# Optimization experiments

Measured on AMD Instinct MI355X. Metric: run time of the kernel, lower is better.

## Reference

```python
import jax, jax.numpy as jnp
import numpy as np

T, B, L, CTX, H = 512, 512, 16, 64, 128
STATE_DIM, SHOT, PID, DATA = 32, 12, 35, 23


def setup_inputs() -> dict:
    key = jax.random.key(0)
    ks = jax.random.split(key, 64)
    k = iter(ks)
    def rn(shape, s=0.1):
        return (jax.random.normal(next(k), shape) * s).astype(jnp.float32)
    xs = jax.random.normal(next(k), (T, B, DATA), jnp.float32)
    xs = xs.at[:, :, 12].set(jax.random.randint(next(k), (T, B), 0, SHOT).astype(jnp.float32))
    xs = xs.at[:, :, 17].set(jax.random.randint(next(k), (T, B), 0, PID).astype(jnp.float32))
    xs = xs.at[:, :, 20].set(jax.random.randint(next(k), (T, B), 0, SHOT).astype(jnp.float32))
    return dict(
        total_xs=jnp.zeros((1,), jnp.float32),
        xs=xs,
        ts=jnp.linspace(0.0, 2.0, T).astype(jnp.float32),
        noise_std=jnp.asarray(0.1, jnp.float32),
        z0_noise=jax.random.normal(next(k), (B, L), jnp.float32),
        bm_noise=jax.random.normal(next(k), (T - 1, B, L), jnp.float32),
        shot_emb=rn((SHOT, 8)), player_emb=rn((PID, 8)),
        gru_wih=rn((3 * H, STATE_DIM)), gru_whh=rn((3 * H, H)),
        gru_bih=rn((3 * H,)), gru_bhh=rn((3 * H,)),
        enc_w=rn((CTX, H)), enc_b=rn((CTX,)),
        qz0_w=rn((2 * L, CTX)), qz0_b=rn((2 * L,)),
        f_w1=rn((H, L + CTX)), f_b1=rn((H,)), f_w2=rn((H, H)), f_b2=rn((H,)),
        f_w3=rn((L, H)), f_b3=rn((L,)),
        h_w1=rn((H, L)), h_b1=rn((H,)), h_w2=rn((H, H)), h_b2=rn((H,)),
        h_w3=rn((L, H)), h_b3=rn((L,)),
        g_w1=rn((L, H)), g_b1=rn((L, H)), g_w2=rn((L, H)), g_b2=rn((L,)),
        proj_w=rn((STATE_DIM, L)), proj_b=rn((STATE_DIM,)),
        pz0_mean=jnp.zeros((1, L), jnp.float32), pz0_logstd=jnp.zeros((1, L), jnp.float32),
        act_w=rn((128, L)), act_b=rn((128,)),
        act_land_w=rn((2, 128)), act_shot_w=rn((SHOT, 128)), act_move_w=rn((2, 128)),
    )


def _forward(xs, noise_std, shot_emb, player_emb, gru_wih, gru_whh, gru_bih, gru_bhh,
             enc_w, enc_b, qz0_w, qz0_b,
             f_w1, f_b1, f_w2, f_b2, f_w3, f_b3,
             h_w1, h_b1, h_w2, h_b2, h_w3, h_b3,
             g_w1, g_b1, g_w2, g_b2,
             proj_w, proj_b, pz0_mean, pz0_logstd,
             act_w, act_b, act_land_w, act_shot_w, act_move_w,
             ts, z0_noise, bm_noise):
    # --- SDE_embed_and_transform: replace shot/player id cols with embeddings ---
    state = xs[:, :, :18]
    shot_ids = state[:, :, 12].astype(jnp.int32)
    pid_ids = state[:, :, 17].astype(jnp.int32)
    state_t = jnp.concatenate([state[:, :, :12], shot_emb[shot_ids],
                               state[:, :, 13:17], player_emb[pid_ids]], axis=-1)  # (T,B,32)
    xs_t = jnp.concatenate([state_t, xs[:, :, 18:]], axis=-1)  # (T,B,37)
    # --- Encoder: GRU over time-reversed states, linear head, flip back ---
    def gru_step(h, xt):
        gi = xt @ gru_wih.T + gru_bih
        gh = h @ gru_whh.T + gru_bhh
        ir, iz, inn = jnp.split(gi, 3, axis=-1)
        hr, hz, hn = jnp.split(gh, 3, axis=-1)
        r = jax.nn.sigmoid(ir + hr)
        zg = jax.nn.sigmoid(iz + hz)
        n = jnp.tanh(inn + r * hn)
        hnew = (1.0 - zg) * n + zg * h
        return hnew, hnew
    h0 = jnp.zeros((xs.shape[1], gru_whh.shape[1]), xs.dtype)
    _, hs = jax.lax.scan(gru_step, h0, state_t[::-1])
    ctx = (hs @ enc_w.T + enc_b)[::-1]  # (T,B,CTX)
    # --- posterior z0 ---
    qm, qls = jnp.split(ctx[0] @ qz0_w.T + qz0_b, 2, axis=1)
    z0 = qm + jnp.exp(qls) * z0_noise
    # --- Euler-Maruyama with logqp; searchsorted(right) -> ctx[min(i+1,T-1)] = ctx[i+1] ---
    dts = ts[1:] - ts[:-1]  # (T-1,)
    dW = jnp.sqrt(dts)[:, None, None] * bm_noise
    ctx_steps = ctx[1:]
    def mlp3(x, w1, b1, w2, b2, w3, b3):
        h1 = jax.nn.softplus(x @ w1.T + b1)
        h2 = jax.nn.softplus(h1 @ w2.T + b2)
        return h2 @ w3.T + b3
    def g_diag(y):  # (B,L): per-latent-dim scalar nets, batched over L
        hg = jax.nn.softplus(y[:, :, None] * g_w1[None] + g_b1[None])  # (B,L,H)
        return jax.nn.sigmoid(jnp.einsum('blh,lh->bl', hg, g_w2) + g_b2)
    def sde_step(z, inp):
        c, dw, dt = inp
        f_val = mlp3(jnp.concatenate([z, c], axis=1), f_w1, f_b1, f_w2, f_b2, f_w3, f_b3)
        h_val = mlp3(z, h_w1, h_b1, h_w2, h_b2, h_w3, h_b3)
        g_val = g_diag(z)
        u = (f_val - h_val) / g_val
        logr = 0.5 * jnp.sum(u * u, axis=1) * dt
        z_new = z + f_val * dt + g_val * dw
        return z_new, (z_new, logr)
    _, (z_tail, log_ratio) = jax.lax.scan(sde_step, z0, (ctx_steps, dW, dts))
    zs = jnp.concatenate([z0[None], z_tail], axis=0)  # (T,B,L)
    _xs = zs @ proj_w.T + proj_b  # (T,B,32)
    # --- action model losses ---
    a = jax.nn.relu(zs @ act_w.T + act_b)
    land = (a @ act_land_w.T).reshape(-1, 2)
    shot_logits = (a @ act_shot_w.T).reshape(-1, act_shot_w.shape[0])
    move = (a @ act_move_w.T).reshape(-1, 2)
    true_actions = xs_t[:, :, -5:]
    true_land = true_actions[:, :, :2].reshape(-1, 2)
    true_move = true_actions[:, :, 3:].reshape(-1, 2)
    true_shot = true_actions[:, :, 2].astype(jnp.int32).reshape(-1)
    land_loss = jnp.mean((land - true_land) ** 2)
    move_loss = jnp.mean((move - true_move) ** 2)
    logp = jax.nn.log_softmax(shot_logits, axis=-1)
    picked = jnp.take_along_axis(logp, true_shot[:, None], axis=1)[:, 0]
    mask = (true_shot != 0).astype(logp.dtype)  # CrossEntropy ignore_index=0
    shot_loss = -jnp.sum(picked * mask) / jnp.maximum(jnp.sum(mask), 1.0)
    # --- reconstruction log-likelihood ---
    xs_state = xs_t[:, :, :STATE_DIM]
    LOG2PI = 1.8378770664093453
    log_pxs = jnp.mean(jnp.sum(
        -0.5 * ((xs_state - _xs) / noise_std) ** 2 - jnp.log(noise_std) - 0.5 * LOG2PI,
        axis=(0, 2)))
    # --- KL(q(z0) || p(z0)) ---
    var_q = jnp.exp(2.0 * qls)
    var_p = jnp.exp(2.0 * pz0_logstd)
    kl = pz0_logstd - qls + (var_q + (qm - pz0_mean) ** 2) / (2.0 * var_p) - 0.5
    logqp0 = jnp.mean(jnp.sum(kl, axis=1))
    logqp_path = jnp.mean(jnp.sum(log_ratio, axis=0))
    return log_pxs, logqp0 + logqp_path + land_loss + shot_loss + move_loss


def reference(total_xs, xs, ts, noise_std, z0_noise, bm_noise, shot_emb, player_emb,
              gru_wih, gru_whh, gru_bih, gru_bhh, enc_w, enc_b, qz0_w, qz0_b,
              f_w1, f_b1, f_w2, f_b2, f_w3, f_b3, h_w1, h_b1, h_w2, h_b2, h_w3, h_b3,
              g_w1, g_b1, g_w2, g_b2, proj_w, proj_b, pz0_mean, pz0_logstd,
              act_w, act_b, act_land_w, act_shot_w, act_move_w):
    return _forward(xs, noise_std, shot_emb, player_emb, gru_wih, gru_whh, gru_bih, gru_bhh,
                    enc_w, enc_b, qz0_w, qz0_b,
                    f_w1, f_b1, f_w2, f_b2, f_w3, f_b3,
                    h_w1, h_b1, h_w2, h_b2, h_w3, h_b3,
                    g_w1, g_b1, g_w2, g_b2,
                    proj_w, proj_b, pz0_mean, pz0_logstd,
                    act_w, act_b, act_land_w, act_shot_w, act_move_w,
                    ts, z0_noise, bm_noise)
```

## Files before the change

kernel.cpp:

```cpp
#include <hip/hip_runtime.h>
#include <cstdint>

typedef _Float16 f16;
typedef _Float16 f16x2 __attribute__((ext_vector_type(2)));

#define T_STEPS 512
#define B_SZ 512
#define LOG2PI 1.8378770664093453f

__device__ __forceinline__ void barrier_lds() {
  asm volatile("s_waitcnt lgkmcnt(0)" ::: "memory");
  __builtin_amdgcn_s_barrier();
  asm volatile("" ::: "memory");
}

__device__ __forceinline__ uint32_t packh2(float a, float b) {
  f16x2 v; v[0] = (f16)a; v[1] = (f16)b;
  return __builtin_bit_cast(uint32_t, v);
}

__device__ __forceinline__ float fdot2(uint32_t a, uint32_t b, float c) {
#if defined(__AMDGCN__) && __has_builtin(__builtin_amdgcn_fdot2)
  return __builtin_amdgcn_fdot2(__builtin_bit_cast(f16x2, a),
                                __builtin_bit_cast(f16x2, b), c, false);
#else
  f16x2 x = __builtin_bit_cast(f16x2, a), y = __builtin_bit_cast(f16x2, b);
  return c + (float)x[0] * (float)y[0] + (float)x[1] * (float)y[1];
#endif
}

#define DOT4(acc, w0, w1, w2, w3, v)                                     \
  do {                                                                   \
    acc = fdot2((w0), (v).x, acc); acc = fdot2((w1), (v).y, acc);        \
    acc = fdot2((w2), (v).z, acc); acc = fdot2((w3), (v).w, acc);        \
  } while (0)

__device__ __forceinline__ float sigmoidf_(float x) {
  return 1.0f / (1.0f + __expf(-x));
}
__device__ __forceinline__ float tanhf_(float x) {
  float ax = fabsf(x);
  float t = __expf(-2.0f * ax);
  float r = (1.0f - t) / (1.0f + t);
  return copysignf(r, x);
}
__device__ __forceinline__ float softplusf_(float x) {
  return fmaxf(x, 0.0f) + __logf(1.0f + __expf(-fabsf(x)));
}

__global__ __launch_bounds__(256) void k_embed(
    const float* __restrict__ xs, const float* __restrict__ shot_emb,
    const float* __restrict__ player_emb, f16* __restrict__ state_t,
    float* __restrict__ accums) {
  if (blockIdx.x == 0 && threadIdx.x < 16) accums[threadIdx.x] = 0.0f;
  size_t idx = (size_t)blockIdx.x * 256 + threadIdx.x;
  const float* xp = xs + idx * 23;
  f16* op = state_t + idx * 32;
  int sid = (int)xp[12];
  int pid = (int)xp[17];
#pragma unroll
  for (int i = 0; i < 12; ++i) op[i] = (f16)xp[i];
  const float* se = shot_emb + sid * 8;
#pragma unroll
  for (int i = 0; i < 8; ++i) op[12 + i] = (f16)se[i];
#pragma unroll
  for (int i = 0; i < 4; ++i) op[20 + i] = (f16)xp[13 + i];
  const float* pe = player_emb + pid * 8;
#pragma unroll
  for (int i = 0; i < 8; ++i) op[24 + i] = (f16)pe[i];
}

__global__ __launch_bounds__(256) void k_gtab(
    const float* __restrict__ gw1, const float* __restrict__ gb1,
    const float* __restrict__ gw2, const float* __restrict__ gb2,
    float* __restrict__ g_tab) {
  int gid = blockIdx.x * 256 + threadIdx.x;
  int l = gid >> 16, yi = gid & 0xffff;
  f16 hy = __builtin_bit_cast(f16, (unsigned short)yi);
  float y = (float)hy;
  const float* w1 = gw1 + l * 128;
  const float* b1 = gb1 + l * 128;
  const float* w2 = gw2 + l * 128;
  float a0 = 0.f, a1 = 0.f;
#pragma unroll 8
  for (int h = 0; h < 128; h += 2) {
    a0 = fmaf(softplusf_(fmaf(y, w1[h], b1[h])), w2[h], a0);
    a1 = fmaf(softplusf_(fmaf(y, w1[h + 1], b1[h + 1])), w2[h + 1], a1);
  }
  g_tab[gid] = sigmoidf_(a0 + a1 + gb2[l]);
}

__global__ __launch_bounds__(512) void k_gru(
    const f16* __restrict__ state_t, const float* __restrict__ wih,
    const float* __restrict__ whh, const float* __restrict__ bih,
    const float* __restrict__ bhh, const float* __restrict__ enc_w,
    const float* __restrict__ enc_b, const float* __restrict__ qz0_w,
    const float* __restrict__ qz0_b, const float* __restrict__ z0_noise,
    const float* __restrict__ pz0_mean, const float* __restrict__ pz0_logstd,
    f16* __restrict__ ctx, float* __restrict__ z0_out,
    float* __restrict__ accums) {
  __shared__ uint32_t s_x[2][16];
  __shared__ uint32_t s_h[2][64];
  __shared__ float s_gates[2 * 128 * 4];
  __shared__ float s_encp[2 * 64 * 2];
  __shared__ float s_ctx0[2][64];
  __shared__ float s_q[2][32];

  const int tid = threadIdx.x;
  const int bbase = blockIdx.x * 2;
  const uint32_t* stu = (const uint32_t*)state_t;

  uint32_t wA[64];
  uint32_t wB[16];
  float bias0 = 0.f, bias1 = 0.f, encbr = 0.f;

  if (tid < 256) {
    int g = tid >> 7, du = tid & 127;
    const float* whr = whh + (size_t)(g * 128 + du) * 128;
#pragma unroll
    for (int i = 0; i < 64; ++i) wA[i] = packh2(whr[2 * i], whr[2 * i + 1]);
    const float* wxr = wih + (size_t)(g * 128 + du) * 32;
#pragma unroll
    for (int i = 0; i < 16; ++i) wB[i] = packh2(wxr[2 * i], wxr[2 * i + 1]);
    bias0 = bih[g * 128 + du] + bhh[g * 128 + du];
  } else if (tid < 384) {
    int du = tid - 256;
    const float* whr = whh + (size_t)(256 + du) * 128;
#pragma unroll
    for (int i = 0; i < 64; ++i) wA[i] = packh2(whr[2 * i], whr[2 * i + 1]);
    const float* wxr = wih + (size_t)(256 + du) * 32;
#pragma unroll
    for (int i = 0; i < 16; ++i) wB[i] = packh2(wxr[2 * i], wxr[2 * i + 1]);
    bias0 = bih[256 + du];
    bias1 = bhh[256 + du];
  } else {
    int e = tid - 384, c = e & 63, ks = e >> 6;
    const float* wer = enc_w + (size_t)c * 128 + ks * 64;
#pragma unroll
    for (int i = 0; i < 32; ++i) wA[i] = packh2(wer[2 * i], wer[2 * i + 1]);
    encbr = enc_b[c];
  }

  if (tid < 128) s_h[tid >> 6][tid & 63] = 0u;
  if (tid < 32) {
    int b = tid >> 4, i = tid & 15;
    s_x[b][i] = stu[((size_t)(T_STEPS - 1) * B_SZ + bbase + b) * 16 + i];
  }
  float h_old = 0.0f;
  __syncthreads();

  for (int t = T_STEPS - 1; t >= 0; --t) {
    uint4 xpref = make_uint4(0, 0, 0, 0);
    if (tid < 256) {
      int g = tid >> 7, du = tid & 127;
#pragma unroll
      for (int b = 0; b < 2; ++b) {
        float a = bias0;
        const uint4* xq = (const uint4*)&s_x[b][0];
#pragma unroll
        for (int j = 0; j < 4; ++j) {
          uint4 v = xq[j];
          DOT4(a, wB[4 * j], wB[4 * j + 1], wB[4 * j + 2], wB[4 * j + 3], v);
        }
        const uint4* hq = (const uint4*)&s_h[b][0];
#pragma unroll
        for (int j = 0; j < 16; ++j) {
          uint4 v = hq[j];
          DOT4(a, wA[4 * j], wA[4 * j + 1], wA[4 * j + 2], wA[4 * j + 3], v);
        }
        s_gates[(b * 128 + du) * 4 + g] = a;
      }
    } else if (tid < 384) {
      int du = tid - 256;
#pragma unroll
      for (int b = 0; b < 2; ++b) {
        float aI = bias0, aH = bias1;
        const uint4* xq = (const uint4*)&s_x[b][0];
#pragma unroll
        for (int j = 0; j < 4; ++j) {
          uint4 v = xq[j];
          DOT4(aI, wB[4 * j], wB[4 * j + 1], wB[4 * j + 2], wB[4 * j + 3], v);
        }
        const uint4* hq = (const uint4*)&s_h[b][0];
#pragma unroll
        for (int j = 0; j < 16; ++j) {
          uint4 v = hq[j];
          DOT4(aH, wA[4 * j], wA[4 * j + 1], wA[4 * j + 2], wA[4 * j + 3], v);
        }
        s_gates[(b * 128 + du) * 4 + 2] = aI;
        s_gates[(b * 128 + du) * 4 + 3] = aH;
      }
    } else {
      int e = tid - 384, ks = e >> 6, cc = e & 63;
      (void)cc;
      if (t < T_STEPS - 1) {
#pragma unroll
        for (int b = 0; b < 2; ++b) {
          float a = 0.f;
          const uint4* hq = (const uint4*)&s_h[b][ks * 32];
#pragma unroll
          for (int j = 0; j < 8; ++j) {
            uint4 v = hq[j];
            DOT4(a, wA[4 * j], wA[4 * j + 1], wA[4 * j + 2], wA[4 * j + 3], v);
          }
          s_encp[(b * 64 + cc) * 2 + ks] = a;
        }
      }
      if (e < 8 && t > 0) {
        int b = e & 1, q = e >> 1;
        xpref = *(const uint4*)(stu +
                                ((size_t)(t - 1) * B_SZ + bbase + b) * 16 + q * 4);
      }
    }
    barrier_lds();
    if (tid < 256) {
      int b = tid >> 7, du = tid & 127;
      const float4 gt = *(const float4*)&s_gates[(b * 128 + du) * 4];
      float r = sigmoidf_(gt.x), zg = sigmoidf_(gt.y);
      float n = tanhf_(gt.z + r * gt.w);
      float hnew = (1.0f - zg) * n + zg * h_old;
      h_old = hnew;
      ((f16*)&s_h[b][0])[du] = (f16)hnew;
    } else if (tid >= 384) {
      int e = tid - 384, cc = e & 63, b = e >> 6;
      if (t < T_STEPS - 1) {
        float2 p = *(const float2*)&s_encp[(b * 64 + cc) * 2];
        ctx[((size_t)(t + 1) * B_SZ + bbase + b) * 64 + cc] =
            (f16)(p.x + p.y + encbr);
      }
      if (e < 8 && t > 0) {
        int b2 = e & 1, q = e >> 1;
        *(uint4*)&s_x[b2][q * 4] = xpref;
      }
    }
    barrier_lds();
  }

  if (tid >= 384) {
    int e = tid - 384, ks = e >> 6, cc = e & 63;
#pragma unroll
    for (int b = 0; b < 2; ++b) {
      float a = 0.f;
      const uint4* hq = (const uint4*)&s_h[b][ks * 32];
#pragma unroll
      for (int j = 0; j < 8; ++j) {
        uint4 v = hq[j];
        DOT4(a, wA[4 * j], wA[4 * j + 1], wA[4 * j + 2], wA[4 * j + 3], v);
      }
      s_encp[(b * 64 + cc) * 2 + ks] = a;
    }
  }
  __syncthreads();
  if (tid >= 384) {
    int e = tid - 384, cc = e & 63, b = e >> 6;
    float2 p = *(const float2*)&s_encp[(b * 64 + cc) * 2];
    float val = p.x + p.y + encbr;
    ctx[((size_t)bbase + b) * 64 + cc] = (f16)val;
    s_ctx0[b][cc] = val;
  }
  __syncthreads();
  if (tid < 64) {
    int b = tid >> 5, o = tid & 31;
    float acc = qz0_b[o];
#pragma unroll 8
    for (int k = 0; k < 64; ++k) acc += qz0_w[o * 64 + k] * s_ctx0[b][k];
    s_q[b][o] = acc;
  }
  __syncthreads();
  if (tid < 32) {
    int b = tid >> 4, l = tid & 15;
    int bg = bbase + b;
    float qm = s_q[b][l], qls = s_q[b][16 + l];
    float z0v = qm + __expf(qls) * z0_noise[bg * 16 + l];
    z0_out[bg * 16 + l] = z0v;
    float pm = pz0_mean[l], pls = pz0_logstd[l];
    float var_q = __expf(2.0f * qls);
    float var_p = __expf(2.0f * pls);
    float dm = qm - pm;
    float kl = pls - qls + (var_q + dm * dm) / (2.0f * var_p) - 0.5f;
    atomicAdd(&accums[5], kl);
  }
}

__global__ __launch_bounds__(256, 2) void k_sde(
    const f16* __restrict__ ctx, const float* __restrict__ z0_in,
    const float* __restrict__ ts, const float* __restrict__ bm_noise,
    const float* __restrict__ fw1, const float* __restrict__ fb1,
    const float* __restrict__ fw2, const float* __restrict__ fb2,
    const float* __restrict__ fw3, const float* __restrict__ fb3,
    const float* __restrict__ hw1, const float* __restrict__ hb1,
    const float* __restrict__ hw2, const float* __restrict__ hb2,
    const float* __restrict__ hw3, const float* __restrict__ hb3,
    const float* __restrict__ g_tab,
    f16* __restrict__ zs, float* __restrict__ accums) {
  __shared__ uint32_t s_x2[2][40];
  __shared__ uint32_t s_h1[2][64];
  __shared__ uint32_t s_h2[2][64];
  __shared__ float s_dts[T_STEPS];

  const int tid = threadIdx.x;
  const int lane = tid & 63;
  const int bg = blockIdx.x;
  const uint4* ctx4 = (const uint4*)ctx;

  const int r1 = tid >> 1, hh = tid & 1;
  const int mlp = tid >> 7, u2 = tid & 127;
  const int r3 = lane >> 1;
  const int net3 = r3 >> 4;
  const int l3 = r3 & 15;
  const int hh3 = lane & 1;
  const bool zlane = (net3 == 0) && (hh3 == 0);
  const bool stg = (tid >= 32 && tid < 40);

  uint32_t uw1f[20], uw1h[4], wP2[64];
  uint4 w3r[8];
  float bf1r, bh1r, bias2r, fb3r, hb3r;
  {
    const float* w = fw1 + (size_t)r1 * 80 + hh * 40;
#pragma unroll
    for (int i = 0; i < 20; ++i) uw1f[i] = packh2(w[2 * i], w[2 * i + 1]);
    bf1r = fb1[r1];
  }
  {
    const float* w = hw1 + (size_t)r1 * 16 + hh * 8;
#pragma unroll
    for (int i = 0; i < 4; ++i) uw1h[i] = packh2(w[2 * i], w[2 * i + 1]);
    bh1r = hb1[r1];
  }
  {
    const float* w = (mlp ? hw2 : fw2) + (size_t)u2 * 128;
#pragma unroll
    for (int i = 0; i < 64; ++i) wP2[i] = packh2(w[2 * i], w[2 * i + 1]);
    bias2r = (mlp ? hb2 : fb2)[u2];
  }
  fb3r = fb3[l3];
  hb3r = hb3[l3];
  {
    const float* w = (net3 ? hw3 : fw3) + (size_t)l3 * 128 + hh3 * 64;
#pragma unroll
    for (int j = 0; j < 8; ++j) {
      uint4 q;
      q.x = packh2(w[8 * j + 0], w[8 * j + 1]);
      q.y = packh2(w[8 * j + 2], w[8 * j + 3]);
      q.z = packh2(w[8 * j + 4], w[8 * j + 5]);
      q.w = packh2(w[8 * j + 6], w[8 * j + 7]);
      w3r[j] = q;
    }
  }
  for (int i = tid; i < T_STEPS - 1; i += 256) s_dts[i] = ts[i + 1] - ts[i];

  float zreg = 0.f, bmc = 0.f, bmn = 0.f, gvp = 0.f, path_acc = 0.f;
  uint4 cpref = make_uint4(0, 0, 0, 0);
  if (zlane) {
    zreg = z0_in[bg * 16 + l3];
    ((f16*)&s_x2[0][0])[l3] = (f16)zreg;
    if (tid < 64) zs[(size_t)bg * 16 + l3] = (f16)zreg;
    bmc = bm_noise[(size_t)bg * 16 + l3];
    bmn = bm_noise[((size_t)1 * B_SZ + bg) * 16 + l3];
    unsigned short zb = __builtin_bit_cast(unsigned short, (f16)zreg);
    gvp = g_tab[l3 * 65536 + (int)zb];
  }
  if (stg) {
    int q = tid - 32;
    uint4 v = ctx4[((size_t)1 * B_SZ + bg) * 8 + q];
    *(uint4*)&s_x2[0][8 + q * 4] = v;
  }
  __syncthreads();

  for (int t = 0; t < T_STEPS - 1; ++t) {
    const int p = t & 1;
    if (stg && t <= T_STEPS - 3)
      cpref = ctx4[((size_t)(t + 2) * B_SZ + bg) * 8 + (tid - 32)];
    if (t > 0) {
      const uint4* hq = (const uint4*)&s_h2[net3][hh3 * 32];
      float a0 = 0.f, a1 = 0.f;
#pragma unroll
      for (int j = 0; j < 8; j += 2) {
        uint4 w0 = w3r[j], w1v = w3r[j + 1];
        uint4 v0 = hq[j], v1 = hq[j + 1];
        DOT4(a0, w0.x, w0.y, w0.z, w0.w, v0);
        DOT4(a1, w1v.x, w1v.y, w1v.z, w1v.w, v1);
      }
      float a = a0 + a1;
      float full = a + __shfl_xor(a, 1);
      float cross = __shfl_xor(full, 32);
      if (zlane) {
        float fv = full + fb3r;
        float hv = cross + hb3r;
        float gv = gvp;
        float dt = s_dts[t - 1];
        float u_ = (fv - hv) / gv;
        float ls = u_ * u_;
        ls += __shfl_xor(ls, 2);
        ls += __shfl_xor(ls, 4);
        ls += __shfl_xor(ls, 8);
        ls += __shfl_xor(ls, 16);
        if (tid == 0) path_acc += 0.5f * ls * dt;
        float dw = sqrtf(dt) * bmc;
        float zn = zreg + fv * dt + gv * dw;
        zreg = zn;
        ((f16*)&s_x2[p][0])[l3] = (f16)zn;
        if (tid < 64) zs[((size_t)t * B_SZ + bg) * 16 + l3] = (f16)zn;
        bmc = bmn;
        if (t <= T_STEPS - 3)
          bmn = bm_noise[((size_t)(t + 1) * B_SZ + bg) * 16 + l3];
        unsigned short zb = __builtin_bit_cast(unsigned short, (f16)zn);
        gvp = g_tab[l3 * 65536 + (int)zb];
      }
    }
    {
      const uint4* xq = (const uint4*)&s_x2[p][0];
      const int base = hh * 5;
      float a0 = 0.f, a1 = 0.f;
      {
        uint4 v0 = xq[base + 0], v1 = xq[base + 1];
        DOT4(a0, uw1f[0], uw1f[1], uw1f[2], uw1f[3], v0);
        DOT4(a1, uw1f[4], uw1f[5], uw1f[6], uw1f[7], v1);
        uint4 v2 = xq[base + 2], v3 = xq[base + 3];
        DOT4(a0, uw1f[8], uw1f[9], uw1f[10], uw1f[11], v2);
        DOT4(a1, uw1f[12], uw1f[13], uw1f[14], uw1f[15], v3);
        uint4 v4 = xq[base + 4];
        DOT4(a0, uw1f[16], uw1f[17], uw1f[18], uw1f[19], v4);
      }
      float af = a0 + a1;
      uint4 vz = xq[hh];
      float ah = 0.f;
      DOT4(ah, uw1h[0], uw1h[1], uw1h[2], uw1h[3], vz);
      float ff = af + __shfl_xor(af, 1);
      float fh = ah + __shfl_xor(ah, 1);
      if (hh == 0)
        ((f16*)&s_h1[0][0])[r1] = (f16)softplusf_(ff + bf1r);
      else
        ((f16*)&s_h1[1][0])[r1] = (f16)softplusf_(fh + bh1r);
    }
    barrier_lds();
    {
      const uint4* hq = (const uint4*)&s_h1[mlp][0];
      float a0 = 0.f, a1 = 0.f;
#pragma unroll
      for (int j = 0; j < 16; j += 2) {
        uint4 v0 = hq[j], v1 = hq[j + 1];
        DOT4(a0, wP2[4 * j], wP2[4 * j + 1], wP2[4 * j + 2], wP2[4 * j + 3], v0);
        DOT4(a1, wP2[4 * j + 4], wP2[4 * j + 5], wP2[4 * j + 6], wP2[4 * j + 7], v1);
      }
      ((f16*)&s_h2[mlp][0])[u2] = (f16)softplusf_(a0 + a1 + bias2r);
    }
    if (stg && t <= T_STEPS - 3)
      *(uint4*)&s_x2[p ^ 1][8 + (tid - 32) * 4] = cpref;
    barrier_lds();
  }

  if (tid < 64) {
    const uint4* hq = (const uint4*)&s_h2[net3][hh3 * 32];
    float a0 = 0.f, a1 = 0.f;
#pragma unroll
    for (int j = 0; j < 8; j += 2) {
      uint4 w0 = w3r[j], w1v = w3r[j + 1];
      uint4 v0 = hq[j], v1 = hq[j + 1];
      DOT4(a0, w0.x, w0.y, w0.z, w0.w, v0);
      DOT4(a1, w1v.x, w1v.y, w1v.z, w1v.w, v1);
    }
    float a = a0 + a1;
    float full = a + __shfl_xor(a, 1);
    float cross = __shfl_xor(full, 32);
    if (zlane) {
      float fv = full + fb3r;
      float hv = cross + hb3r;
      float gv = gvp;
      float dt = s_dts[T_STEPS - 2];
      float u_ = (fv - hv) / gv;
      float ls = u_ * u_;
      ls += __shfl_xor(ls, 2);
      ls += __shfl_xor(ls, 4);
      ls += __shfl_xor(ls, 8);
      ls += __shfl_xor(ls, 16);
      if (tid == 0) path_acc += 0.5f * ls * dt;
      float dw = sqrtf(dt) * bmc;
      float zn = zreg + fv * dt + gv * dw;
      zs[((size_t)(T_STEPS - 1) * B_SZ + bg) * 16 + l3] = (f16)zn;
    }
  }
  if (tid == 0) atomicAdd(&accums[6], path_acc);
}

__global__ __launch_bounds__(256) void k_dec(
    const f16* __restrict__ zs, const f16* __restrict__ state_t,
    const float* __restrict__ xs, const float* __restrict__ proj_w,
    const float* __restrict__ proj_b, const float* __restrict__ act_w,
    const float* __restrict__ act_b, const float* __restrict__ land_w,
    const float* __restrict__ shot_w, const float* __restrict__ move_w,
    float* __restrict__ accums) {
  __shared__ uint32_t s_proj[8 * 32];
  __shared__ uint32_t s_act[8 * 128];
  __shared__ uint32_t s_head[128 * 8];
  __shared__ float s_pb[32], s_ab[128];
  __shared__ float s_red[4 * 5];

  const int tid = threadIdx.x;
  for (int id = tid; id < 8 * 32; id += 256) {
    int kp = id & 7, n = id >> 3;
    s_proj[kp * 32 + n] = packh2(proj_w[n * 16 + 2 * kp], proj_w[n * 16 + 2 * kp + 1]);
  }
  for (int id = tid; id < 8 * 128; id += 256) {
    int kp = id & 7, n = id >> 3;
    s_act[kp * 128 + n] = packh2(act_w[n * 16 + 2 * kp], act_w[n * 16 + 2 * kp + 1]);
  }
  for (int id = tid; id < 128 * 8; id += 256) {
    int j = id >> 3, p = id & 7;
    int h0 = 2 * p, h1 = 2 * p + 1;
    float w0 = (h0 < 2) ? land_w[h0 * 128 + j]
                        : (h0 < 14 ? shot_w[(h0 - 2) * 128 + j]
                                   : move_w[(h0 - 14) * 128 + j]);
    float w1 = (h1 < 2) ? land_w[h1 * 128 + j]
                        : (h1 < 14 ? shot_w[(h1 - 2) * 128 + j]
                                   : move_w[(h1 - 14) * 128 + j]);
    s_head[j * 8 + p] = packh2(w0, w1);
  }
  if (tid < 32) s_pb[tid] = proj_b[tid];
  if (tid < 128) s_ab[tid] = act_b[tid];
  __syncthreads();

  size_t idx = (size_t)blockIdx.x * 256 + tid;
  uint32_t z2[8];
  const uint32_t* zp = (const uint32_t*)(zs + idx * 16);
#pragma unroll
  for (int i = 0; i < 8; ++i) z2[i] = zp[i];
  uint32_t stv[16];
  const uint32_t* stp = (const uint32_t*)(state_t + idx * 32);
#pragma unroll
  for (int i = 0; i < 16; ++i) stv[i] = stp[i];

  float sqsum = 0.0f;
#pragma unroll 4
  for (int i = 0; i < 32; ++i) {
    float acc = s_pb[i];
#pragma unroll
    for (int kp = 0; kp < 8; ++kp) acc = fdot2(s_proj[kp * 32 + i], z2[kp], acc);
    f16x2 sv = __builtin_bit_cast(f16x2, stv[i >> 1]);
    float d = (float)sv[i & 1] - acc;
    sqsum += d * d;
  }

  float hd[16];
#pragma unroll
  for (int i = 0; i < 16; ++i) hd[i] = 0.0f;
#pragma unroll 2
  for (int j = 0; j < 128; ++j) {
    float a = s_ab[j];
#pragma unroll
    for (int kp = 0; kp < 8; ++kp) a = fdot2(s_act[kp * 128 + j], z2[kp], a);
    a = fmaxf(a, 0.0f);
#pragma unroll
    for (int p = 0; p < 8; ++p) {
      f16x2 w = __builtin_bit_cast(f16x2, s_head[j * 8 + p]);
      hd[2 * p] += (float)w[0] * a;
      hd[2 * p + 1] += (float)w[1] * a;
    }
  }
  const float* xp = xs + idx * 23;
  float dl0 = hd[0] - xp[18], dl1 = hd[1] - xp[19];
  float land = dl0 * dl0 + dl1 * dl1;
  float dm0 = hd[14] - xp[21], dm1 = hd[15] - xp[22];
  float move = dm0 * dm0 + dm1 * dm1;
  int sid = (int)xp[20];
  float m = hd[2];
#pragma unroll
  for (int s = 1; s < 12; ++s) m = fmaxf(m, hd[2 + s]);
  float sume = 0.0f;
#pragma unroll
  for (int s = 0; s < 12; ++s) sume += __expf(hd[2 + s] - m);
  float lse = m + __logf(sume);
  float pl = 0.0f;
#pragma unroll
  for (int s = 0; s < 12; ++s)
    if (s == sid) pl = hd[2 + s];
  float picked = 0.0f, cnt = 0.0f;
  if (sid != 0) {
    picked = pl - lse;
    cnt = 1.0f;
  }
  float vals[5] = {sqsum, land, move, picked, cnt};
#pragma unroll
  for (int v = 0; v < 5; ++v) {
    float x = vals[v];
    for (int off = 1; off < 64; off <<= 1) x += __shfl_xor(x, off);
    vals[v] = x;
  }
  int lane = tid & 63, wv = tid >> 6;
  if (lane == 0) {
#pragma unroll
    for (int v = 0; v < 5; ++v) s_red[wv * 5 + v] = vals[v];
  }
  __syncthreads();
  if (tid == 0) {
#pragma unroll
    for (int v = 0; v < 5; ++v) {
      float s = s_red[v] + s_red[5 + v] + s_red[10 + v] + s_red[15 + v];
      atomicAdd(&accums[v], s);
    }
  }
}

__global__ void k_fin(const float* __restrict__ accums,
                      const float* __restrict__ noise_std,
                      float* __restrict__ out) {
  if (threadIdx.x == 0 && blockIdx.x == 0) {
    float sd = noise_std[0];
    float log_pxs = -0.5f * accums[0] / (sd * sd * (float)B_SZ) -
                    (float)T_STEPS * 32.0f * (logf(sd) + 0.5f * LOG2PI);
    float land = accums[1] / (float)(T_STEPS * B_SZ * 2);
    float move = accums[2] / (float)(T_STEPS * B_SZ * 2);
    float shot = -accums[3] / fmaxf(accums[4], 1.0f);
    float out1 = accums[5] / (float)B_SZ + accums[6] / (float)B_SZ + land + shot + move;
    out[0] = log_pxs;
    out[1] = out1;
  }
}

extern "C" void kernel_launch(void* const* d_in, const int* in_sizes, int n_in,
                              void* d_out, int out_size, void* d_ws,
                              size_t ws_size, hipStream_t stream) {
  const float* xs = (const float*)d_in[1];
  const float* ts = (const float*)d_in[2];
  const float* noise_std = (const float*)d_in[3];
  const float* z0_noise = (const float*)d_in[4];
  const float* bm_noise = (const float*)d_in[5];
  const float* shot_emb = (const float*)d_in[6];
  const float* player_emb = (const float*)d_in[7];
  const float* gru_wih = (const float*)d_in[8];
  const float* gru_whh = (const float*)d_in[9];
  const float* gru_bih = (const float*)d_in[10];
  const float* gru_bhh = (const float*)d_in[11];
  const float* enc_w = (const float*)d_in[12];
  const float* enc_b = (const float*)d_in[13];
  const float* qz0_w = (const float*)d_in[14];
  const float* qz0_b = (const float*)d_in[15];
  const float* f_w1 = (const float*)d_in[16];
  const float* f_b1 = (const float*)d_in[17];
  const float* f_w2 = (const float*)d_in[18];
  const float* f_b2 = (const float*)d_in[19];
  const float* f_w3 = (const float*)d_in[20];
  const float* f_b3 = (const float*)d_in[21];
  const float* h_w1 = (const float*)d_in[22];
  const float* h_b1 = (const float*)d_in[23];
  const float* h_w2 = (const float*)d_in[24];
  const float* h_b2 = (const float*)d_in[25];
  const float* h_w3 = (const float*)d_in[26];
  const float* h_b3 = (const float*)d_in[27];
  const float* g_w1 = (const float*)d_in[28];
  const float* g_b1 = (const float*)d_in[29];
  const float* g_w2 = (const float*)d_in[30];
  const float* g_b2 = (const float*)d_in[31];
  const float* proj_w = (const float*)d_in[32];
  const float* proj_b = (const float*)d_in[33];
  const float* pz0_mean = (const float*)d_in[34];
  const float* pz0_logstd = (const float*)d_in[35];
  const float* act_w = (const float*)d_in[36];
  const float* act_b = (const float*)d_in[37];
  const float* act_land_w = (const float*)d_in[38];
  const float* act_shot_w = (const float*)d_in[39];
  const float* act_move_w = (const float*)d_in[40];

  char* ws = (char*)d_ws;
  float* accums = (float*)ws;
  f16* state_t = (f16*)(ws + 256);
  f16* ctx = (f16*)(ws + 256 + 16777216);
  float* z0b = (float*)(ws + 256 + 16777216 + 33554432);
  f16* zs = (f16*)(ws + 256 + 16777216 + 33554432 + 32768);
  float* g_tab = (float*)(ws + 256 + 16777216 + 33554432 + 32768 + 8388608);

  k_embed<<<1024, 256, 0, stream>>>(xs, shot_emb, player_emb, state_t, accums);
  k_gtab<<<4096, 256, 0, stream>>>(g_w1, g_b1, g_w2, g_b2, g_tab);
  k_gru<<<256, 512, 0, stream>>>(state_t, gru_wih, gru_whh, gru_bih, gru_bhh,
                                 enc_w, enc_b, qz0_w, qz0_b, z0_noise, pz0_mean,
                                 pz0_logstd, ctx, z0b, accums);
  k_sde<<<512, 256, 0, stream>>>(ctx, z0b, ts, bm_noise, f_w1, f_b1, f_w2, f_b2,
                                 f_w3, f_b3, h_w1, h_b1, h_w2, h_b2, h_w3, h_b3,
                                 g_tab, zs, accums);
  k_dec<<<1024, 256, 0, stream>>>(zs, state_t, xs, proj_w, proj_b, act_w, act_b,
                                  act_land_w, act_shot_w, act_move_w, accums);
  k_fin<<<1, 64, 0, stream>>>(accums, noise_std, (float*)d_out);
}
```

Measured before the change: 1.737 ms.

## Spread SDE layer-3 across two waves as a third phase per step

The third MLP layer and the Euler update are moved out of the step preamble into their own phase after layer 2. That phase runs on 128 threads (two wavefronts), with each output split four ways instead of two. The context buffer becomes single-buffered, written in the same phase by threads in another wave, and the g-table and noise loads move to the start of each step. This shortens the per-step serial dot-product chain, at the cost of a third barrier per timestep and exposed g_tab latency at the start of each step.

```diff
diff --git a/kernel.cpp b/kernel.cpp
--- a/kernel.cpp
+++ b/kernel.cpp
@@ -293,28 +293,26 @@
     const float* __restrict__ hw3, const float* __restrict__ hb3,
     const float* __restrict__ g_tab,
     f16* __restrict__ zs, float* __restrict__ accums) {
-  __shared__ uint32_t s_x2[2][40];
+  __shared__ uint32_t s_x2[40];
   __shared__ uint32_t s_h1[2][64];
   __shared__ uint32_t s_h2[2][64];
   __shared__ float s_dts[T_STEPS];
 
   const int tid = threadIdx.x;
-  const int lane = tid & 63;
   const int bg = blockIdx.x;
   const uint4* ctx4 = (const uint4*)ctx;
 
   const int r1 = tid >> 1, hh = tid & 1;
-  const int mlp = tid >> 7, u2 = tid & 127;
-  const int r3 = lane >> 1;
-  const int net3 = r3 >> 4;
-  const int l3 = r3 & 15;
-  const int hh3 = lane & 1;
-  const bool zlane = (net3 == 0) && (hh3 == 0);
-  const bool stg = (tid >= 32 && tid < 40);
-
-  uint32_t uw1f[20], uw1h[4], wP2[64];
-  uint4 w3r[8];
-  float bf1r, bh1r, bias2r, fb3r, hb3r;
+  const int mlp2 = tid >> 7, u2 = tid & 127;
+  const int l3 = (tid >> 3) & 15;
+  const int mlp3 = (tid >> 2) & 1;
+  const int kq = tid & 3;
+  const bool p3act = (tid < 128);
+  const bool zlane = p3act && ((tid & 7) == 0);
+  const bool stg = (tid >= 128 && tid < 136);
+
+  uint32_t uw1f[20], uw1h[4], wP2[64], wP3[16];
+  float bf1r, bh1r, bias2r, fb3r = 0.f, hb3r = 0.f;
   {
     const float* w = fw1 + (size_t)r1 * 80 + hh * 40;
 #pragma unroll
@@ -328,88 +326,48 @@
     bh1r = hb1[r1];
   }
   {
-    const float* w = (mlp ? hw2 : fw2) + (size_t)u2 * 128;
+    const float* w = (mlp2 ? hw2 : fw2) + (size_t)u2 * 128;
 #pragma unroll
     for (int i = 0; i < 64; ++i) wP2[i] = packh2(w[2 * i], w[2 * i + 1]);
-    bias2r = (mlp ? hb2 : fb2)[u2];
-  }
-  fb3r = fb3[l3];
-  hb3r = hb3[l3];
-  {
-    const float* w = (net3 ? hw3 : fw3) + (size_t)l3 * 128 + hh3 * 64;
-#pragma unroll
-    for (int j = 0; j < 8; ++j) {
-      uint4 q;
-      q.x = packh2(w[8 * j + 0], w[8 * j + 1]);
-      q.y = packh2(w[8 * j + 2], w[8 * j + 3]);
-      q.z = packh2(w[8 * j + 4], w[8 * j + 5]);
-      q.w = packh2(w[8 * j + 6], w[8 * j + 7]);
-      w3r[j] = q;
-    }
+    bias2r = (mlp2 ? hb2 : fb2)[u2];
+  }
+  if (p3act) {
+    const float* w = (mlp3 ? hw3 : fw3) + (size_t)l3 * 128 + kq * 32;
+#pragma unroll
+    for (int i = 0; i < 16; ++i) wP3[i] = packh2(w[2 * i], w[2 * i + 1]);
+    fb3r = fb3[l3];
+    hb3r = hb3[l3];
   }
   for (int i = tid; i < T_STEPS - 1; i += 256) s_dts[i] = ts[i + 1] - ts[i];
 
-  float zreg = 0.f, bmc = 0.f, bmn = 0.f, gvp = 0.f, path_acc = 0.f;
+  float zreg = 0.f, bmc = 0.f, path_acc = 0.f;
   uint4 cpref = make_uint4(0, 0, 0, 0);
   if (zlane) {
     zreg = z0_in[bg * 16 + l3];
-    ((f16*)&s_x2[0][0])[l3] = (f16)zreg;
-    if (tid < 64) zs[(size_t)bg * 16 + l3] = (f16)zreg;
+    ((f16*)&s_x2[0])[l3] = (f16)zreg;
+    zs[(size_t)bg * 16 + l3] = (f16)zreg;
     bmc = bm_noise[(size_t)bg * 16 + l3];
-    bmn = bm_noise[((size_t)1 * B_SZ + bg) * 16 + l3];
-    unsigned short zb = __builtin_bit_cast(unsigned short, (f16)zreg);
-    gvp = g_tab[l3 * 65536 + (int)zb];
   }
   if (stg) {
-    int q = tid - 32;
+    int q = tid - 128;
     uint4 v = ctx4[((size_t)1 * B_SZ + bg) * 8 + q];
-    *(uint4*)&s_x2[0][8 + q * 4] = v;
+    *(uint4*)&s_x2[8 + q * 4] = v;
   }
   __syncthreads();
 
   for (int t = 0; t < T_STEPS - 1; ++t) {
-    const int p = t & 1;
+    float bmn = 0.f, gvp = 0.f;
+    if (zlane) {
+      unsigned short zb = __builtin_bit_cast(unsigned short, (f16)zreg);
+      gvp = g_tab[l3 * 65536 + (int)zb];
+      if (t < T_STEPS - 2)
+        bmn = bm_noise[((size_t)(t + 1) * B_SZ + bg) * 16 + l3];
+    }
     if (stg && t <= T_STEPS - 3)
-      cpref = ctx4[((size_t)(t + 2) * B_SZ + bg) * 8 + (tid - 32)];
-    if (t > 0) {
-      const uint4* hq = (const uint4*)&s_h2[net3][hh3 * 32];
-      float a0 = 0.f, a1 = 0.f;
-#pragma unroll
-      for (int j = 0; j < 8; j += 2) {
-        uint4 w0 = w3r[j], w1v = w3r[j + 1];
-        uint4 v0 = hq[j], v1 = hq[j + 1];
-        DOT4(a0, w0.x, w0.y, w0.z, w0.w, v0);
-        DOT4(a1, w1v.x, w1v.y, w1v.z, w1v.w, v1);
-      }
-      float a = a0 + a1;
-      float full = a + __shfl_xor(a, 1);
-      float cross = __shfl_xor(full, 32);
-      if (zlane) {
-        float fv = full + fb3r;
-        float hv = cross + hb3r;
-        float gv = gvp;
-        float dt = s_dts[t - 1];
-        float u_ = (fv - hv) / gv;
-        float ls = u_ * u_;
-        ls += __shfl_xor(ls, 2);
-        ls += __shfl_xor(ls, 4);
-        ls += __shfl_xor(ls, 8);
-        ls += __shfl_xor(ls, 16);
-        if (tid == 0) path_acc += 0.5f * ls * dt;
-        float dw = sqrtf(dt) * bmc;
-        float zn = zreg + fv * dt + gv * dw;
-        zreg = zn;
-        ((f16*)&s_x2[p][0])[l3] = (f16)zn;
-        if (tid < 64) zs[((size_t)t * B_SZ + bg) * 16 + l3] = (f16)zn;
-        bmc = bmn;
-        if (t <= T_STEPS - 3)
-          bmn = bm_noise[((size_t)(t + 1) * B_SZ + bg) * 16 + l3];
-        unsigned short zb = __builtin_bit_cast(unsigned short, (f16)zn);
-        gvp = g_tab[l3 * 65536 + (int)zb];
-      }
-    }
+      cpref = ctx4[((size_t)(t + 2) * B_SZ + bg) * 8 + (tid - 128)];
+
     {
-      const uint4* xq = (const uint4*)&s_x2[p][0];
+      const uint4* xq = (const uint4*)&s_x2[0];
       const int base = hh * 5;
       float a0 = 0.f, a1 = 0.f;
       {
@@ -435,7 +393,7 @@
     }
     barrier_lds();
     {
-      const uint4* hq = (const uint4*)&s_h1[mlp][0];
+      const uint4* hq = (const uint4*)&s_h1[mlp2][0];
       float a0 = 0.f, a1 = 0.f;
 #pragma unroll
       for (int j = 0; j < 16; j += 2) {
@@ -443,44 +401,46 @@
         DOT4(a0, wP2[4 * j], wP2[4 * j + 1], wP2[4 * j + 2], wP2[4 * j + 3], v0);
         DOT4(a1, wP2[4 * j + 4], wP2[4 * j + 5], wP2[4 * j + 6], wP2[4 * j + 7], v1);
       }
-      ((f16*)&s_h2[mlp][0])[u2] = (f16)softplusf_(a0 + a1 + bias2r);
-    }
-    if (stg && t <= T_STEPS - 3)
-      *(uint4*)&s_x2[p ^ 1][8 + (tid - 32) * 4] = cpref;
+      ((f16*)&s_h2[mlp2][0])[u2] = (f16)softplusf_(a0 + a1 + bias2r);
+    }
     barrier_lds();
-  }
-
-  if (tid < 64) {
-    const uint4* hq = (const uint4*)&s_h2[net3][hh3 * 32];
-    float a0 = 0.f, a1 = 0.f;
-#pragma unroll
-    for (int j = 0; j < 8; j += 2) {
-      uint4 w0 = w3r[j], w1v = w3r[j + 1];
-      uint4 v0 = hq[j], v1 = hq[j + 1];
-      DOT4(a0, w0.x, w0.y, w0.z, w0.w, v0);
-      DOT4(a1, w1v.x, w1v.y, w1v.z, w1v.w, v1);
-    }
-    float a = a0 + a1;
-    float full = a + __shfl_xor(a, 1);
-    float cross = __shfl_xor(full, 32);
-    if (zlane) {
-      float fv = full + fb3r;
-      float hv = cross + hb3r;
-      float gv = gvp;
-      float dt = s_dts[T_STEPS - 2];
-      float u_ = (fv - hv) / gv;
-      float ls = u_ * u_;
-      ls += __shfl_xor(ls, 2);
-      ls += __shfl_xor(ls, 4);
-      ls += __shfl_xor(ls, 8);
-      ls += __shfl_xor(ls, 16);
-      if (tid == 0) path_acc += 0.5f * ls * dt;
-      float dw = sqrtf(dt) * bmc;
-      float zn = zreg + fv * dt + gv * dw;
-      zs[((size_t)(T_STEPS - 1) * B_SZ + bg) * 16 + l3] = (f16)zn;
-    }
-  }
-  if (tid == 0) atomicAdd(&accums[6], path_acc);
+    if (p3act) {
+      const uint4* hq = (const uint4*)&s_h2[mlp3][kq * 16];
+      float a0 = 0.f, a1 = 0.f;
+#pragma unroll
+      for (int j = 0; j < 4; j += 2) {
+        uint4 v0 = hq[j], v1 = hq[j + 1];
+        DOT4(a0, wP3[4 * j], wP3[4 * j + 1], wP3[4 * j + 2], wP3[4 * j + 3], v0);
+        DOT4(a1, wP3[4 * j + 4], wP3[4 * j + 5], wP3[4 * j + 6], wP3[4 * j + 7], v1);
+      }
+      float a = a0 + a1;
+      float s1 = a + __shfl_xor(a, 1);
+      float s2 = s1 + __shfl_xor(s1, 2);
+      float other = __shfl_xor(s2, 4);
+      if ((tid & 7) == 0) {
+        float fv = s2 + fb3r;
+        float hv = other + hb3r;
+        float gv = gvp;
+        float dt = s_dts[t];
+        float u_ = (fv - hv) / gv;
+        float ls = u_ * u_;
+        ls += __shfl_xor(ls, 8);
+        ls += __shfl_xor(ls, 16);
+        ls += __shfl_xor(ls, 32);
+        if ((tid & 63) == 0) path_acc += 0.5f * ls * dt;
+        float dw = sqrtf(dt) * bmc;
+        float zn = zreg + fv * dt + gv * dw;
+        zreg = zn;
+        ((f16*)&s_x2[0])[l3] = (f16)zn;
+        zs[((size_t)(t + 1) * B_SZ + bg) * 16 + l3] = (f16)zn;
+        bmc = bmn;
+      }
+    } else if (stg && t <= T_STEPS - 3) {
+      *(uint4*)&s_x2[8 + (tid - 128) * 4] = cpref;
+    }
+    barrier_lds();
+  }
+  if (tid == 0 || tid == 64) atomicAdd(&accums[6], path_acc);
 }
 
 __global__ __launch_bounds__(256) void k_dec(
```

Result: faster. 1.632 ms (-6.0%).
